# Performance work log

Measured on AMD Instinct MI355X. Metric: run time of the kernel, lower is better.

## Reference

```python
import jax, jax.numpy as jnp
import numpy as np

N_NODES = 100000
N_EDGES = 1600000
DIM_IN, DIM_HID, DIM_OUT = 256, 128, 64


def _gcn_norm(edge_index, num_nodes):
    # PyG gcn_norm with add_self_loops=True, symmetric normalization.
    loop = jnp.arange(num_nodes, dtype=edge_index.dtype)
    row = jnp.concatenate([edge_index[0], loop])  # source
    col = jnp.concatenate([edge_index[1], loop])  # destination
    deg = jax.ops.segment_sum(jnp.ones_like(col, dtype=jnp.float32), col,
                              num_segments=num_nodes)
    dis = jnp.where(deg > 0, jax.lax.rsqrt(deg), 0.0)
    norm = dis[row] * dis[col]  # [E + N]
    return row, col, norm


def _gcn_conv(x, row, col, norm, W, b, num_nodes):
    h = x @ W                      # [N, d_out] linear first (d_out <= d_in typical)
    msg = h[row] * norm[:, None]   # gather + edge scaling, [E+N, d_out]
    out = jax.ops.segment_sum(msg, col, num_segments=num_nodes)  # scatter-add
    return out + b


def setup_inputs() -> dict:
    key = jax.random.key(0)
    k1, k2, k3, k4, k5 = jax.random.split(key, 5)
    x = jax.random.normal(k1, (N_NODES, DIM_IN), dtype=jnp.float32)
    edge_index = jax.random.randint(k2, (2, N_EDGES), 0, N_NODES, dtype=jnp.int32)
    s1 = 1.0 / np.sqrt(DIM_IN)
    s2 = 1.0 / np.sqrt(DIM_HID)
    W1 = jax.random.uniform(k3, (DIM_IN, DIM_HID), jnp.float32, -s1, s1)
    b1 = jnp.zeros((DIM_HID,), jnp.float32)
    W2 = jax.random.uniform(k4, (DIM_HID, DIM_OUT), jnp.float32, -s2, s2)
    b2 = jnp.zeros((DIM_OUT,), jnp.float32)
    return {"x": x, "edge_index": edge_index, "W1": W1, "b1": b1,
            "W2": W2, "b2": b2}


def reference(x, edge_index, W1, b1, W2, b2):
    n = x.shape[0]
    row, col, norm = _gcn_norm(edge_index, n)  # cached=True: shared by both layers
    h = _gcn_conv(x, row, col, norm, W1, b1, n)
    h = jax.nn.relu(h)
    h = _gcn_conv(h, row, col, norm, W2, b2, n)
    return jax.nn.log_softmax(h, axis=-1)
```

## Files before the change

kernel.cpp:

```cpp
#include <hip/hip_runtime.h>

#define N_NODES 100000
#define N_EDGES 1600000
#define DIN 256
#define DHID 128
#define DOUT 64

#define BSHIFT 8
#define NBUCKET ((N_NODES + 255) / 256)
#define CHUNK 4096
#define NCHUNK ((N_EDGES + CHUNK - 1) / CHUNK)

typedef __attribute__((ext_vector_type(8))) short bf16x8;
typedef __attribute__((ext_vector_type(4))) float f32x4;
typedef __attribute__((ext_vector_type(2))) float f32x2;

static __device__ __forceinline__ ushort f2bf(float f) {
  union { float f; uint u; } a; a.f = f;
  uint u = a.u;
  uint r = u + 0x7fffu + ((u >> 16) & 1u);
  return (ushort)(r >> 16);
}


#if __has_builtin(__builtin_amdgcn_cvt_pk_f32_fp8) && __has_builtin(__builtin_amdgcn_cvt_pk_fp8_f32) && __has_builtin(__builtin_amdgcn_cvt_f32_fp8)
#define FP8_HW 1
#else
#define FP8_HW 0
#endif

static __device__ __forceinline__ uint f2fp8(float f) {
#if FP8_HW
  return (uint)(__builtin_amdgcn_cvt_pk_fp8_f32(f, f, 0, false) & 0xFF);
#else
  uint u = __float_as_uint(f);
  uint s = (u >> 24) & 0x80u;
  u &= 0x7FFFFFFFu;
  u += 0x7FFFFu + ((u >> 20) & 1u);
  int e = (int)(u >> 23) - 120;
  uint m = (u >> 20) & 7u;
  uint v = (e <= 0) ? 0u : ((e >= 15) ? 0x7Eu : (((uint)e << 3) | m));
  return s | v;
#endif
}

static __device__ __forceinline__ f32x2 fp8x2f(uint v) {
#if FP8_HW
  return __builtin_amdgcn_cvt_pk_f32_fp8(v, false);
#else
  uint lo = v & 0xFFu, hi = (v >> 8) & 0xFFu;
  uint mlo = lo & 0x7Fu, mhi = hi & 0x7Fu;
  uint blo = (mlo ? ((mlo << 4) + 0x3C00u) : 0u) | ((lo & 0x80u) << 8);
  uint bhi = (mhi ? ((mhi << 4) + 0x3C00u) : 0u) | ((hi & 0x80u) << 8);
  f32x2 r;
  r.x = __uint_as_float(blo << 16);
  r.y = __uint_as_float(bhi << 16);
  return r;
#endif
}


__global__ __launch_bounds__(256) void k_hist(const int* __restrict__ colp,
                                              int* __restrict__ cntmat) {
  __shared__ int h[NBUCKET];
  int c = blockIdx.x;
  for (int i = threadIdx.x; i < NBUCKET; i += 256) h[i] = 0;
  __syncthreads();
  int e0 = c * CHUNK, e1 = min(e0 + CHUNK, N_EDGES);
  for (int e = e0 + threadIdx.x; e < e1; e += 256)
    atomicAdd(&h[colp[e] >> BSHIFT], 1);
  __syncthreads();
  for (int i = threadIdx.x; i < NBUCKET; i += 256)
    cntmat[c * NBUCKET + i] = h[i];
}


__global__ __launch_bounds__(256) void k_buckettot(const int* __restrict__ cntmat,
                                                   int* __restrict__ btot) {
  __shared__ int s[256];
  int b = blockIdx.x, t = threadIdx.x;
  int sum = 0;
  for (int c = t; c < NCHUNK; c += 256) sum += cntmat[c * NBUCKET + b];
  s[t] = sum;
  __syncthreads();
  for (int d = 128; d > 0; d >>= 1) {
    if (t < d) s[t] += s[t + d];
    __syncthreads();
  }
  if (t == 0) btot[b] = s[0];
}


__global__ __launch_bounds__(256) void k_chunkpfx(const int* __restrict__ cntmat,
                                                  const int* __restrict__ btot,
                                                  int* __restrict__ bbase,
                                                  int* __restrict__ basemat) {
  __shared__ int s[256];
  __shared__ int bb[NBUCKET + 1];
  int t = threadIdx.x;
  int b0 = 2 * t, b1 = 2 * t + 1;
  int v0 = (b0 < NBUCKET) ? btot[b0] : 0;
  int v1 = (b1 < NBUCKET) ? btot[b1] : 0;
  int ps = v0 + v1;
  s[t] = ps;
  __syncthreads();
  for (int d = 1; d < 256; d <<= 1) {
    int y = (t >= d) ? s[t - d] : 0;
    __syncthreads();
    s[t] += y;
    __syncthreads();
  }
  int ex = s[t] - ps;
  if (b0 < NBUCKET) bb[b0] = ex;
  if (b1 < NBUCKET) bb[b1] = ex + v0;
  if (t == 0) bb[NBUCKET] = N_EDGES;
  __syncthreads();
  if (blockIdx.x == 0) {
    for (int i = t; i <= NBUCKET; i += 256) bbase[i] = bb[i];
  }
  int wid = blockIdx.x * 4 + (t >> 6);
  int lane = t & 63;
  if (wid >= NBUCKET) return;
  int carry = bb[wid];
  const int NT = (NCHUNK + 63) / 64;
  for (int tt = 0; tt < NT; tt++) {
    int c = tt * 64 + lane;
    int v = (c < NCHUNK) ? cntmat[c * NBUCKET + wid] : 0;
    int incl = v;
#pragma unroll
    for (int d = 1; d < 64; d <<= 1) {
      int y = __shfl_up(incl, d, 64);
      if (lane >= d) incl += y;
    }
    if (c < NCHUNK) basemat[c * NBUCKET + wid] = carry + incl - v;
    carry += __shfl(incl, 63, 64);
  }
}


__global__ __launch_bounds__(256) void k_binscatter(const int* __restrict__ rowp,
                                                    const int* __restrict__ colp,
                                                    const int* __restrict__ basemat,
                                                    uint* __restrict__ packed) {
  __shared__ int lcur[NBUCKET];
  int c = blockIdx.x;
  for (int i = threadIdx.x; i < NBUCKET; i += 256)
    lcur[i] = basemat[c * NBUCKET + i];
  __syncthreads();
  int e0 = c * CHUNK, e1 = min(e0 + CHUNK, N_EDGES);
  for (int e = e0 + threadIdx.x; e < e1; e += 256) {
    int dst = colp[e], src = rowp[e];
    int pos = atomicAdd(&lcur[dst >> BSHIFT], 1);
    packed[pos] = (uint)src | ((uint)(dst & 255) << 17);
  }
}


__global__ __launch_bounds__(256) void k_count256(const uint* __restrict__ packed,
                                                  const int* __restrict__ bbase,
                                                  int* __restrict__ off,
                                                  float* __restrict__ dis) {
  __shared__ int cnt[256];
  __shared__ int s[256];
  int b = blockIdx.x, t = threadIdx.x;
  int node0 = b << BSHIFT;
  int nn = min(256, N_NODES - node0);
  cnt[t] = 0;
  __syncthreads();
  int r0 = bbase[b], r1 = bbase[b + 1];
  for (int r = r0 + t; r < r1; r += 256)
    atomicAdd(&cnt[packed[r] >> 17], 1);
  __syncthreads();
  int c = cnt[t];
  s[t] = c;
  __syncthreads();
  for (int d = 1; d < 256; d <<= 1) {
    int y = (t >= d) ? s[t - d] : 0;
    __syncthreads();
    s[t] += y;
    __syncthreads();
  }
  int ex = s[t] - c;
  if (t < nn) {
    off[node0 + t] = r0 + ex;
    dis[node0 + t] = rsqrtf((float)c + 1.0f);
  }
  if (b == NBUCKET - 1 && t == 0) off[N_NODES] = N_EDGES;
}


__global__ __launch_bounds__(256) void k_place(const uint* __restrict__ packed,
                                               const int* __restrict__ bbase,
                                               const int* __restrict__ off,
                                               const float* __restrict__ dis,
                                               uint* __restrict__ ep) {
  __shared__ int cur[256];
  __shared__ int offl[256];
  int b = blockIdx.x, t = threadIdx.x;
  int node0 = b << BSHIFT;
  int nn = min(256, N_NODES - node0);
  cur[t] = 0;
  if (t < nn) offl[t] = off[node0 + t];
  __syncthreads();
  int r0 = bbase[b], r1 = bbase[b + 1];
  for (int r = r0 + t; r < r1; r += 256) {
    uint sd = packed[r];
    int d0 = sd >> 17;
    uint src = sd & 0x1FFFFu;
    float w = dis[src];
    uint w15 = min((uint)(w * 32768.0f + 0.5f), 32767u);
    int pos = offl[d0] + atomicAdd(&cur[d0], 1);
    ep[pos] = src | (w15 << 17);
  }
}


__global__ void k_packW(const float* __restrict__ W1, ushort* __restrict__ Wp1,
                        const float* __restrict__ W2, ushort* __restrict__ Wp2) {
  int t = blockIdx.x * 256 + threadIdx.x;
  if (t < 8 * 8 * 64) {
    int l = t & 63, ks = (t >> 6) & 7, nt = t >> 9;
    int k0 = ks * 32 + (l >> 4) * 8;
    int n = nt * 16 + (l & 15);
    ushort* dst = Wp1 + (size_t)t * 8;
#pragma unroll
    for (int i = 0; i < 8; i++) dst[i] = f2bf(W1[(k0 + i) * DHID + n]);
  } else if (t < 8 * 8 * 64 + 4 * 4 * 64) {
    int t2 = t - 8 * 8 * 64;
    int l = t2 & 63, ks = (t2 >> 6) & 3, nt = t2 >> 8;
    int k0 = ks * 32 + (l >> 4) * 8;
    int n = nt * 16 + (l & 15);
    ushort* dst = Wp2 + (size_t)t2 * 8;
#pragma unroll
    for (int i = 0; i < 8; i++) dst[i] = f2bf(W2[(k0 + i) * DOUT + n]);
  }
}


__global__ __launch_bounds__(256) void k_gemm1(const float* __restrict__ x,
                                               const ushort* __restrict__ Wp,
                                               uchar* __restrict__ h1) {
  __shared__ uchar cs[4][16][144];
  int w = threadIdx.x >> 6, l = threadIdx.x & 63;
  int row0 = blockIdx.x * 64 + w * 16;
  bool valid = (row0 < N_NODES);
  if (valid) {
    f32x4 acc[8];
#pragma unroll
    for (int i = 0; i < 8; i++) acc[i] = (f32x4)(0.f);
    int arow = row0 + (l & 15);
    const float4* xg = (const float4*)(x + (size_t)arow * DIN) + (l >> 4) * 2;
    const bf16x8* wp = (const bf16x8*)Wp;
    float4 a[16];
#pragma unroll
    for (int ks = 0; ks < 8; ks++) {
      a[2 * ks]     = xg[ks * 8];
      a[2 * ks + 1] = xg[ks * 8 + 1];
    }
#pragma unroll
    for (int ks = 0; ks < 8; ks++) {
      float4 a0 = a[2 * ks];
      float4 a1 = a[2 * ks + 1];
      bf16x8 af;
      af[0] = (short)f2bf(a0.x); af[1] = (short)f2bf(a0.y);
      af[2] = (short)f2bf(a0.z); af[3] = (short)f2bf(a0.w);
      af[4] = (short)f2bf(a1.x); af[5] = (short)f2bf(a1.y);
      af[6] = (short)f2bf(a1.z); af[7] = (short)f2bf(a1.w);
#pragma unroll
      for (int nt = 0; nt < 8; nt++) {
        bf16x8 bf = wp[(nt * 8 + ks) * 64 + l];
        acc[nt] = __builtin_amdgcn_mfma_f32_16x16x32_bf16(af, bf, acc[nt], 0, 0, 0);
      }
    }
#pragma unroll
    for (int nt = 0; nt < 8; nt++)
#pragma unroll
      for (int r = 0; r < 4; r++)
        cs[w][(l >> 4) * 4 + r][nt * 16 + (l & 15)] = (uchar)f2fp8(acc[nt][r]);
  }
  __syncthreads();
  if (valid) {
    const uint4* s4 = (const uint4*)&cs[w][l >> 2][(l & 3) * 32];
    uint4* dst = (uint4*)(h1 + (size_t)(row0 + (l >> 2)) * DHID + (l & 3) * 32);
    dst[0] = s4[0]; dst[1] = s4[1];
  }
}


#define AGG1_BATCH4(eX, pfx)                                                    \
  {                                                                             \
    uint p0 = ep[eX], p1 = ep[eX + 1], p2 = ep[eX + 2], p3 = ep[eX + 3];        \
    ushort v0 = h1[(size_t)(p0 & 0x1FFFFu) * 64 + lane];                        \
    ushort v1 = h1[(size_t)(p1 & 0x1FFFFu) * 64 + lane];                        \
    ushort v2 = h1[(size_t)(p2 & 0x1FFFFu) * 64 + lane];                        \
    ushort v3 = h1[(size_t)(p3 & 0x1FFFFu) * 64 + lane];                        \
    f32x2 f0 = fp8x2f(v0), f1 = fp8x2f(v1), f2 = fp8x2f(v2), f3 = fp8x2f(v3);   \
    float w0 = (float)(p0 >> 17);                                               \
    float w1 = (float)(p1 >> 17);                                               \
    float w2 = (float)(p2 >> 17);                                               \
    float w3 = (float)(p3 >> 17);                                               \
    ax##pfx = fmaf(f0.x, w0, ax##pfx); ay##pfx = fmaf(f0.y, w0, ay##pfx);       \
    ax##pfx = fmaf(f1.x, w1, ax##pfx); ay##pfx = fmaf(f1.y, w1, ay##pfx);       \
    ax##pfx = fmaf(f2.x, w2, ax##pfx); ay##pfx = fmaf(f2.y, w2, ay##pfx);       \
    ax##pfx = fmaf(f3.x, w3, ax##pfx); ay##pfx = fmaf(f3.y, w3, ay##pfx);       \
  }

#define AGG1_TAIL(eX, eX1, pfx)                                                 \
  for (; eX < eX1; eX++) {                                                      \
    uint p = ep[eX];                                                            \
    f32x2 f0 = fp8x2f(h1[(size_t)(p & 0x1FFFFu) * 64 + lane]);                  \
    float w0 = (float)(p >> 17);                                                \
    ax##pfx = fmaf(f0.x, w0, ax##pfx); ay##pfx = fmaf(f0.y, w0, ay##pfx);       \
  }

__global__ __launch_bounds__(256) void k_agg1g2(const ushort* __restrict__ h1,
                                                const int* __restrict__ off,
                                                const uint* __restrict__ ep,
                                                const float* __restrict__ dis,
                                                const float* __restrict__ b1,
                                                const ushort* __restrict__ Wp2,
                                                uchar* __restrict__ h2) {
  __shared__ ushort as[16][136];
  int w = threadIdx.x >> 6, lane = threadIdx.x & 63;
  int nb0 = blockIdx.x * 16;
  float2 bb = ((const float2*)b1)[lane];
  int widA = nb0 + w * 4;
  float dA = dis[widA], dB = dis[widA + 1], dC = dis[widA + 2], dD = dis[widA + 3];
  f32x2 hvA = fp8x2f(h1[(size_t)widA * 64 + lane]);
  f32x2 hvB = fp8x2f(h1[(size_t)(widA + 1) * 64 + lane]);
  f32x2 hvC = fp8x2f(h1[(size_t)(widA + 2) * 64 + lane]);
  f32x2 hvD = fp8x2f(h1[(size_t)(widA + 3) * 64 + lane]);
  float sA = dA * 32768.0f, sB = dB * 32768.0f, sC = dC * 32768.0f, sD = dD * 32768.0f;
  float axA = hvA.x * sA, ayA = hvA.y * sA;
  float axB = hvB.x * sB, ayB = hvB.y * sB;
  float axC = hvC.x * sC, ayC = hvC.y * sC;
  float axD = hvD.x * sD, ayD = hvD.y * sD;
  int eA  = __builtin_amdgcn_readfirstlane(off[widA]);
  int eA1 = __builtin_amdgcn_readfirstlane(off[widA + 1]);
  int eB  = eA1;
  int eB1 = __builtin_amdgcn_readfirstlane(off[widA + 2]);
  int eC  = eB1;
  int eC1 = __builtin_amdgcn_readfirstlane(off[widA + 3]);
  int eD  = eC1;
  int eD1 = __builtin_amdgcn_readfirstlane(off[widA + 4]);
  while (eA + 4 <= eA1 && eB + 4 <= eB1 && eC + 4 <= eC1 && eD + 4 <= eD1) {
    AGG1_BATCH4(eA, A)
    AGG1_BATCH4(eB, B)
    AGG1_BATCH4(eC, C)
    AGG1_BATCH4(eD, D)
    eA += 4; eB += 4; eC += 4; eD += 4;
  }
  while (eA + 4 <= eA1 && eB + 4 <= eB1) {
    AGG1_BATCH4(eA, A)
    AGG1_BATCH4(eB, B)
    eA += 4; eB += 4;
  }
  while (eC + 4 <= eC1 && eD + 4 <= eD1) {
    AGG1_BATCH4(eC, C)
    AGG1_BATCH4(eD, D)
    eC += 4; eD += 4;
  }
  for (; eA + 4 <= eA1; eA += 4) AGG1_BATCH4(eA, A)
  for (; eB + 4 <= eB1; eB += 4) AGG1_BATCH4(eB, B)
  for (; eC + 4 <= eC1; eC += 4) AGG1_BATCH4(eC, C)
  for (; eD + 4 <= eD1; eD += 4) AGG1_BATCH4(eD, D)
  AGG1_TAIL(eA, eA1, A)
  AGG1_TAIL(eB, eB1, B)
  AGG1_TAIL(eC, eC1, C)
  AGG1_TAIL(eD, eD1, D)
  {
    float rx, ry;
    float fA = dA * 0x1p-15f, fB = dB * 0x1p-15f, fC = dC * 0x1p-15f, fD = dD * 0x1p-15f;
    rx = fmaxf(fmaf(fA, axA, bb.x), 0.f); ry = fmaxf(fmaf(fA, ayA, bb.y), 0.f);
    ((uint*)&as[w * 4 + 0][0])[lane] = (uint)f2bf(rx) | ((uint)f2bf(ry) << 16);
    rx = fmaxf(fmaf(fB, axB, bb.x), 0.f); ry = fmaxf(fmaf(fB, ayB, bb.y), 0.f);
    ((uint*)&as[w * 4 + 1][0])[lane] = (uint)f2bf(rx) | ((uint)f2bf(ry) << 16);
    rx = fmaxf(fmaf(fC, axC, bb.x), 0.f); ry = fmaxf(fmaf(fC, ayC, bb.y), 0.f);
    ((uint*)&as[w * 4 + 2][0])[lane] = (uint)f2bf(rx) | ((uint)f2bf(ry) << 16);
    rx = fmaxf(fmaf(fD, axD, bb.x), 0.f); ry = fmaxf(fmaf(fD, ayD, bb.y), 0.f);
    ((uint*)&as[w * 4 + 3][0])[lane] = (uint)f2bf(rx) | ((uint)f2bf(ry) << 16);
  }
  __syncthreads();
  f32x4 acc = (f32x4)(0.f);
  const bf16x8* wp = (const bf16x8*)Wp2;
#pragma unroll
  for (int ks = 0; ks < 4; ks++) {
    bf16x8 af = *(const bf16x8*)&as[lane & 15][ks * 32 + (lane >> 4) * 8];
    bf16x8 bf = wp[(w * 4 + ks) * 64 + lane];
    acc = __builtin_amdgcn_mfma_f32_16x16x32_bf16(af, bf, acc, 0, 0, 0);
  }
#pragma unroll
  for (int r = 0; r < 4; r++) {
    int row = (lane >> 4) * 4 + r;
    h2[(size_t)(nb0 + row) * DOUT + w * 16 + (lane & 15)] = (uchar)f2fp8(acc[r]);
  }
}


#define AGG2_BATCH4(eX)                                                         \
  {                                                                             \
    uint p0 = ep[eX], p1 = ep[eX + 1], p2 = ep[eX + 2], p3 = ep[eX + 3];        \
    uint v0 = h2u[(size_t)(p0 & 0x1FFFFu) * 16 + q];                            \
    uint v1 = h2u[(size_t)(p1 & 0x1FFFFu) * 16 + q];                            \
    uint v2 = h2u[(size_t)(p2 & 0x1FFFFu) * 16 + q];                            \
    uint v3 = h2u[(size_t)(p3 & 0x1FFFFu) * 16 + q];                            \
    float w0 = (float)(p0 >> 17);                                               \
    float w1 = (float)(p1 >> 17);                                               \
    float w2 = (float)(p2 >> 17);                                               \
    float w3 = (float)(p3 >> 17);                                               \
    f32x2 l0 = fp8x2f(v0), h0 = fp8x2f(v0 >> 16);                               \
    f32x2 l1 = fp8x2f(v1), h1_ = fp8x2f(v1 >> 16);                              \
    f32x2 l2 = fp8x2f(v2), h2_ = fp8x2f(v2 >> 16);                              \
    f32x2 l3 = fp8x2f(v3), h3_ = fp8x2f(v3 >> 16);                              \
    a0 = fmaf(l0.x, w0, a0); a1 = fmaf(l0.y, w0, a1);                           \
    a2 = fmaf(h0.x, w0, a2); a3 = fmaf(h0.y, w0, a3);                           \
    a0 = fmaf(l1.x, w1, a0); a1 = fmaf(l1.y, w1, a1);                           \
    a2 = fmaf(h1_.x, w1, a2); a3 = fmaf(h1_.y, w1, a3);                         \
    a0 = fmaf(l2.x, w2, a0); a1 = fmaf(l2.y, w2, a1);                           \
    a2 = fmaf(h2_.x, w2, a2); a3 = fmaf(h2_.y, w2, a3);                         \
    a0 = fmaf(l3.x, w3, a0); a1 = fmaf(l3.y, w3, a1);                           \
    a2 = fmaf(h3_.x, w3, a2); a3 = fmaf(h3_.y, w3, a3);                         \
  }

__global__ __launch_bounds__(256) void k_agg2(const uint* __restrict__ h2u,
                                              const int* __restrict__ off,
                                              const uint* __restrict__ ep,
                                              const float* __restrict__ dis,
                                              const float* __restrict__ b2,
                                              float* __restrict__ out) {
  int gw   = (blockIdx.x * 256 + threadIdx.x) >> 6;
  int lane = threadIdx.x & 63;
  int g = lane >> 4;
  int q = lane & 15;
  int wid = gw * 4 + g;
  if (wid >= N_NODES) return;
  float d = dis[wid];
  uint sv = h2u[(size_t)wid * 16 + q];
  f32x2 slo = fp8x2f(sv), shi = fp8x2f(sv >> 16);
  float dS = d * 32768.0f;
  float a0 = slo.x * dS, a1 = slo.y * dS, a2 = shi.x * dS, a3 = shi.y * dS;
  int o0 = off[wid], o1 = off[wid + 1];
  int e = o0;
  for (; e + 4 <= o1; e += 4) AGG2_BATCH4(e)
  for (; e < o1; e++) {
    uint p = ep[e];
    uint v = h2u[(size_t)(p & 0x1FFFFu) * 16 + q];
    float w = (float)(p >> 17);
    f32x2 lo = fp8x2f(v), hi = fp8x2f(v >> 16);
    a0 = fmaf(lo.x, w, a0); a1 = fmaf(lo.y, w, a1);
    a2 = fmaf(hi.x, w, a2); a3 = fmaf(hi.y, w, a3);
  }
  float4 bbv = ((const float4*)b2)[q];
  float ds = d * 0x1p-15f;
  float v0 = fmaf(ds, a0, bbv.x);
  float v1 = fmaf(ds, a1, bbv.y);
  float v2 = fmaf(ds, a2, bbv.z);
  float v3 = fmaf(ds, a3, bbv.w);
  float m = fmaxf(fmaxf(v0, v1), fmaxf(v2, v3));
#pragma unroll
  for (int sft = 8; sft >= 1; sft >>= 1) m = fmaxf(m, __shfl_xor(m, sft, 64));
  float sum = expf(v0 - m) + expf(v1 - m) + expf(v2 - m) + expf(v3 - m);
#pragma unroll
  for (int sft = 8; sft >= 1; sft >>= 1) sum += __shfl_xor(sum, sft, 64);
  float ls = m + logf(sum);
  float4 o;
  o.x = v0 - ls; o.y = v1 - ls; o.z = v2 - ls; o.w = v3 - ls;
  ((float4*)out)[(size_t)wid * 16 + q] = o;
}


extern "C" void kernel_launch(void* const* d_in, const int* in_sizes, int n_in,
                              void* d_out, int out_size, void* d_ws, size_t ws_size,
                              hipStream_t stream) {
  const float* x  = (const float*)d_in[0];
  const int*   ei = (const int*)d_in[1];
  const float* W1 = (const float*)d_in[2];
  const float* b1 = (const float*)d_in[3];
  const float* W2 = (const float*)d_in[4];
  const float* b2 = (const float*)d_in[5];
  float* out = (float*)d_out;
  const int* rowp = ei;
  const int* colp = ei + N_EDGES;

  char* p = (char*)d_ws;
  size_t o = 0;
  auto alloc = [&](size_t bytes) -> void* {
    void* r = p + o;
    o = (o + bytes + 255) & ~(size_t)255;
    return r;
  };
  int*    off    = (int*)alloc((size_t)(N_NODES + 1) * 4);
  float*  dis    = (float*)alloc((size_t)N_NODES * 4);
  int*    cntmat = (int*)alloc((size_t)NCHUNK * NBUCKET * 4);
  int*    basemat= (int*)alloc((size_t)NCHUNK * NBUCKET * 4);
  int*    btot   = (int*)alloc((size_t)NBUCKET * 4);
  int*    bbase  = (int*)alloc((size_t)(NBUCKET + 1) * 4);
  uint*   packed = (uint*)alloc((size_t)N_EDGES * 4);
  uint*   ep     = (uint*)alloc((size_t)N_EDGES * 4);
  ushort* Wp1    = (ushort*)alloc((size_t)8 * 8 * 64 * 8 * 2);
  ushort* Wp2    = (ushort*)alloc((size_t)4 * 4 * 64 * 8 * 2);
  uchar*  h1     = (uchar*)alloc((size_t)N_NODES * DHID);
  uchar*  h2     = (uchar*)alloc((size_t)N_NODES * DOUT);

  k_hist<<<NCHUNK, 256, 0, stream>>>(colp, cntmat);
  k_buckettot<<<NBUCKET, 256, 0, stream>>>(cntmat, btot);
  k_chunkpfx<<<(NBUCKET + 3) / 4, 256, 0, stream>>>(cntmat, btot, bbase, basemat);
  k_binscatter<<<NCHUNK, 256, 0, stream>>>(rowp, colp, basemat, packed);
  k_count256<<<NBUCKET, 256, 0, stream>>>(packed, bbase, off, dis);
  k_place<<<NBUCKET, 256, 0, stream>>>(packed, bbase, off, dis, ep);
  k_packW<<<20, 256, 0, stream>>>(W1, Wp1, W2, Wp2);
  k_gemm1<<<(N_NODES + 63) / 64, 256, 0, stream>>>(x, Wp1, h1);
  k_agg1g2<<<N_NODES / 16, 256, 0, stream>>>((const ushort*)h1, off, ep, dis, b1, Wp2, h2);
  k_agg2<<<N_NODES / 16, 256, 0, stream>>>((const uint*)h2, off, ep, dis, b2, out);
}
```

Baseline: 157.8 us.

## Spread GEMM1 blocks across the graph-preprocessing kernels to fill idle CUs

The standalone first-layer GEMM kernel is removed. Its 1563 row-tiles are split into four slices appended as extra blocks to the histogram, bin-scatter, count and place kernels, which each launch only about 391 blocks. The weight-packing kernel moves to the front so the packed weights exist before those kernels run. The aim is to fill CUs left idle by the small, latency-bound CSR-building kernels and to save a launch. In exchange, every one of those kernels now reserves the GEMM staging buffer in shared memory, and the two kinds of block compete for bandwidth.

Result: no change. 154.9 us (-1.8%).

```diff
diff --git a/kernel.cpp b/kernel.cpp
--- a/kernel.cpp
+++ b/kernel.cpp
@@ -10,6 +10,12 @@
 #define NBUCKET ((N_NODES + 255) / 256)
 #define CHUNK 4096
 #define NCHUNK ((N_EDGES + CHUNK - 1) / CHUNK)
+
+#define GEMM1_NB ((N_NODES + 63) / 64)
+#define G_HIST 350
+#define G_BINS 600
+#define G_CNT  300
+#define G_PLC  313
 
 typedef __attribute__((ext_vector_type(8))) short bf16x8;
 typedef __attribute__((ext_vector_type(4))) float f32x4;
@@ -60,9 +66,67 @@
 }
 
 
-__global__ __launch_bounds__(256) void k_hist(const int* __restrict__ colp,
-                                              int* __restrict__ cntmat) {
+static __device__ __forceinline__ void gemm1_body(int gb, const float* __restrict__ x,
+                                                  const ushort* __restrict__ Wp,
+                                                  uchar* __restrict__ h1,
+                                                  uchar (*cs)[16][144]) {
+  int w = threadIdx.x >> 6, l = threadIdx.x & 63;
+  int row0 = gb * 64 + w * 16;
+  bool valid = (row0 < N_NODES);
+  if (valid) {
+    f32x4 acc[8];
+#pragma unroll
+    for (int i = 0; i < 8; i++) acc[i] = (f32x4)(0.f);
+    int arow = row0 + (l & 15);
+    const float4* xg = (const float4*)(x + (size_t)arow * DIN) + (l >> 4) * 2;
+    const bf16x8* wp = (const bf16x8*)Wp;
+    float4 a[16];
+#pragma unroll
+    for (int ks = 0; ks < 8; ks++) {
+      a[2 * ks]     = xg[ks * 8];
+      a[2 * ks + 1] = xg[ks * 8 + 1];
+    }
+#pragma unroll
+    for (int ks = 0; ks < 8; ks++) {
+      float4 a0 = a[2 * ks];
+      float4 a1 = a[2 * ks + 1];
+      bf16x8 af;
+      af[0] = (short)f2bf(a0.x); af[1] = (short)f2bf(a0.y);
+      af[2] = (short)f2bf(a0.z); af[3] = (short)f2bf(a0.w);
+      af[4] = (short)f2bf(a1.x); af[5] = (short)f2bf(a1.y);
+      af[6] = (short)f2bf(a1.z); af[7] = (short)f2bf(a1.w);
+#pragma unroll
+      for (int nt = 0; nt < 8; nt++) {
+        bf16x8 bf = wp[(nt * 8 + ks) * 64 + l];
+        acc[nt] = __builtin_amdgcn_mfma_f32_16x16x32_bf16(af, bf, acc[nt], 0, 0, 0);
+      }
+    }
+#pragma unroll
+    for (int nt = 0; nt < 8; nt++)
+#pragma unroll
+      for (int r = 0; r < 4; r++)
+        cs[w][(l >> 4) * 4 + r][nt * 16 + (l & 15)] = (uchar)f2fp8(acc[nt][r]);
+  }
+  __syncthreads();
+  if (valid) {
+    const uint4* s4 = (const uint4*)&cs[w][l >> 2][(l & 3) * 32];
+    uint4* dst = (uint4*)(h1 + (size_t)(row0 + (l >> 2)) * DHID + (l & 3) * 32);
+    dst[0] = s4[0]; dst[1] = s4[1];
+  }
+}
+
+
+__global__ __launch_bounds__(256) void k_hist_g(const int* __restrict__ colp,
+                                                int* __restrict__ cntmat,
+                                                const float* __restrict__ x,
+                                                const ushort* __restrict__ Wp,
+                                                uchar* __restrict__ h1) {
   __shared__ int h[NBUCKET];
+  __shared__ uchar cs[4][16][144];
+  if (blockIdx.x >= NCHUNK) {
+    gemm1_body(blockIdx.x - NCHUNK + 0, x, Wp, h1, cs);
+    return;
+  }
   int c = blockIdx.x;
   for (int i = threadIdx.x; i < NBUCKET; i += 256) h[i] = 0;
   __syncthreads();
@@ -138,11 +202,19 @@
 }
 
 
-__global__ __launch_bounds__(256) void k_binscatter(const int* __restrict__ rowp,
-                                                    const int* __restrict__ colp,
-                                                    const int* __restrict__ basemat,
-                                                    uint* __restrict__ packed) {
+__global__ __launch_bounds__(256) void k_binscatter_g(const int* __restrict__ rowp,
+                                                      const int* __restrict__ colp,
+                                                      const int* __restrict__ basemat,
+                                                      uint* __restrict__ packed,
+                                                      const float* __restrict__ x,
+                                                      const ushort* __restrict__ Wp,
+                                                      uchar* __restrict__ h1) {
   __shared__ int lcur[NBUCKET];
+  __shared__ uchar cs[4][16][144];
+  if (blockIdx.x >= NCHUNK) {
+    gemm1_body(blockIdx.x - NCHUNK + G_HIST, x, Wp, h1, cs);
+    return;
+  }
   int c = blockIdx.x;
   for (int i = threadIdx.x; i < NBUCKET; i += 256)
     lcur[i] = basemat[c * NBUCKET + i];
@@ -156,12 +228,20 @@
 }
 
 
-__global__ __launch_bounds__(256) void k_count256(const uint* __restrict__ packed,
-                                                  const int* __restrict__ bbase,
-                                                  int* __restrict__ off,
-                                                  float* __restrict__ dis) {
+__global__ __launch_bounds__(256) void k_count256_g(const uint* __restrict__ packed,
+                                                    const int* __restrict__ bbase,
+                                                    int* __restrict__ off,
+                                                    float* __restrict__ dis,
+                                                    const float* __restrict__ x,
+                                                    const ushort* __restrict__ Wp,
+                                                    uchar* __restrict__ h1) {
   __shared__ int cnt[256];
   __shared__ int s[256];
+  __shared__ uchar cs[4][16][144];
+  if (blockIdx.x >= NBUCKET) {
+    gemm1_body(blockIdx.x - NBUCKET + G_HIST + G_BINS, x, Wp, h1, cs);
+    return;
+  }
   int b = blockIdx.x, t = threadIdx.x;
   int node0 = b << BSHIFT;
   int nn = min(256, N_NODES - node0);
@@ -189,13 +269,21 @@
 }
 
 
-__global__ __launch_bounds__(256) void k_place(const uint* __restrict__ packed,
-                                               const int* __restrict__ bbase,
-                                               const int* __restrict__ off,
-                                               const float* __restrict__ dis,
-                                               uint* __restrict__ ep) {
+__global__ __launch_bounds__(256) void k_place_g(const uint* __restrict__ packed,
+                                                 const int* __restrict__ bbase,
+                                                 const int* __restrict__ off,
+                                                 const float* __restrict__ dis,
+                                                 uint* __restrict__ ep,
+                                                 const float* __restrict__ x,
+                                                 const ushort* __restrict__ Wp,
+                                                 uchar* __restrict__ h1) {
   __shared__ int cur[256];
   __shared__ int offl[256];
+  __shared__ uchar cs[4][16][144];
+  if (blockIdx.x >= NBUCKET) {
+    gemm1_body(blockIdx.x - NBUCKET + G_HIST + G_BINS + G_CNT, x, Wp, h1, cs);
+    return;
+  }
   int b = blockIdx.x, t = threadIdx.x;
   int node0 = b << BSHIFT;
   int nn = min(256, N_NODES - node0);
@@ -233,56 +321,6 @@
     ushort* dst = Wp2 + (size_t)t2 * 8;
 #pragma unroll
     for (int i = 0; i < 8; i++) dst[i] = f2bf(W2[(k0 + i) * DOUT + n]);
-  }
-}
-
-
-__global__ __launch_bounds__(256) void k_gemm1(const float* __restrict__ x,
-                                               const ushort* __restrict__ Wp,
-                                               uchar* __restrict__ h1) {
-  __shared__ uchar cs[4][16][144];
-  int w = threadIdx.x >> 6, l = threadIdx.x & 63;
-  int row0 = blockIdx.x * 64 + w * 16;
-  bool valid = (row0 < N_NODES);
-  if (valid) {
-    f32x4 acc[8];
-#pragma unroll
-    for (int i = 0; i < 8; i++) acc[i] = (f32x4)(0.f);
-    int arow = row0 + (l & 15);
-    const float4* xg = (const float4*)(x + (size_t)arow * DIN) + (l >> 4) * 2;
-    const bf16x8* wp = (const bf16x8*)Wp;
-    float4 a[16];
-#pragma unroll
-    for (int ks = 0; ks < 8; ks++) {
-      a[2 * ks]     = xg[ks * 8];
-      a[2 * ks + 1] = xg[ks * 8 + 1];
-    }
-#pragma unroll
-    for (int ks = 0; ks < 8; ks++) {
-      float4 a0 = a[2 * ks];
-      float4 a1 = a[2 * ks + 1];
-      bf16x8 af;
-      af[0] = (short)f2bf(a0.x); af[1] = (short)f2bf(a0.y);
-      af[2] = (short)f2bf(a0.z); af[3] = (short)f2bf(a0.w);
-      af[4] = (short)f2bf(a1.x); af[5] = (short)f2bf(a1.y);
-      af[6] = (short)f2bf(a1.z); af[7] = (short)f2bf(a1.w);
-#pragma unroll
-      for (int nt = 0; nt < 8; nt++) {
-        bf16x8 bf = wp[(nt * 8 + ks) * 64 + l];
-        acc[nt] = __builtin_amdgcn_mfma_f32_16x16x32_bf16(af, bf, acc[nt], 0, 0, 0);
-      }
-    }
-#pragma unroll
-    for (int nt = 0; nt < 8; nt++)
-#pragma unroll
-      for (int r = 0; r < 4; r++)
-        cs[w][(l >> 4) * 4 + r][nt * 16 + (l & 15)] = (uchar)f2fp8(acc[nt][r]);
-  }
-  __syncthreads();
-  if (valid) {
-    const uint4* s4 = (const uint4*)&cs[w][l >> 2][(l & 3) * 32];
-    uint4* dst = (uint4*)(h1 + (size_t)(row0 + (l >> 2)) * DHID + (l & 3) * 32);
-    dst[0] = s4[0]; dst[1] = s4[1];
   }
 }
 
@@ -502,14 +540,13 @@
   uchar*  h1     = (uchar*)alloc((size_t)N_NODES * DHID);
   uchar*  h2     = (uchar*)alloc((size_t)N_NODES * DOUT);
 
-  k_hist<<<NCHUNK, 256, 0, stream>>>(colp, cntmat);
+  k_packW<<<20, 256, 0, stream>>>(W1, Wp1, W2, Wp2);
+  k_hist_g<<<NCHUNK + G_HIST, 256, 0, stream>>>(colp, cntmat, x, Wp1, h1);
   k_buckettot<<<NBUCKET, 256, 0, stream>>>(cntmat, btot);
   k_chunkpfx<<<(NBUCKET + 3) / 4, 256, 0, stream>>>(cntmat, btot, bbase, basemat);
-  k_binscatter<<<NCHUNK, 256, 0, stream>>>(rowp, colp, basemat, packed);
-  k_count256<<<NBUCKET, 256, 0, stream>>>(packed, bbase, off, dis);
-  k_place<<<NBUCKET, 256, 0, stream>>>(packed, bbase, off, dis, ep);
-  k_packW<<<20, 256, 0, stream>>>(W1, Wp1, W2, Wp2);
-  k_gemm1<<<(N_NODES + 63) / 64, 256, 0, stream>>>(x, Wp1, h1);
+  k_binscatter_g<<<NCHUNK + G_BINS, 256, 0, stream>>>(rowp, colp, basemat, packed, x, Wp1, h1);
+  k_count256_g<<<NBUCKET + G_CNT, 256, 0, stream>>>(packed, bbase, off, dis, x, Wp1, h1);
+  k_place_g<<<NBUCKET + G_PLC, 256, 0, stream>>>(packed, bbase, off, dis, ep, x, Wp1, h1);
   k_agg1g2<<<N_NODES / 16, 256, 0, stream>>>((const ushort*)h1, off, ep, dis, b1, Wp2, h2);
   k_agg2<<<N_NODES / 16, 256, 0, stream>>>((const uint*)h2, off, ep, dis, b2, out);
 }
```
